# Kernel tuning notes

Hardware: AMD Instinct MI355X
Metric: run time of the kernel (lower is better)

Reference implementation:

```python
import jax, jax.numpy as jnp
import numpy as np

B, S, H = 2, 2048, 2048
NH, NKV, HD = 16, 4, 128
THETA = 10000.0


def _rope_cos_sin(seq_len, head_dim, theta, dtype):
    inv_freq = 1.0 / (theta ** (jnp.arange(0, head_dim, 2, dtype=jnp.float32) / head_dim))
    t = jnp.arange(seq_len, dtype=jnp.float32)
    freqs = t[:, None] * inv_freq[None, :]          # [S, HD/2]
    emb = jnp.concatenate([freqs, freqs], axis=-1)  # [S, HD]
    return jnp.cos(emb).astype(dtype), jnp.sin(emb).astype(dtype)


def _rotate_half(x):
    d = x.shape[-1] // 2
    return jnp.concatenate([-x[..., d:], x[..., :d]], axis=-1)


def setup_inputs() -> dict:
    key = jax.random.key(0)
    ks = jax.random.split(key, 5)
    x = jax.random.normal(ks[0], (B, S, H), dtype=jnp.float32)
    Wq = jax.random.normal(ks[1], (NH * HD, H), dtype=jnp.float32) * 0.02
    Wk = jax.random.normal(ks[2], (NKV * HD, H), dtype=jnp.float32) * 0.02
    Wv = jax.random.normal(ks[3], (NKV * HD, H), dtype=jnp.float32) * 0.02
    Wo = jax.random.normal(ks[4], (H, H), dtype=jnp.float32) * 0.02
    causal = jnp.tril(jnp.ones((S, S), dtype=bool))
    attention_mask = jnp.where(causal, 0.0, -1e9).astype(jnp.float32)[None, None]  # [1,1,S,S]
    return {"x": x, "attention_mask": attention_mask, "Wq": Wq, "Wk": Wk, "Wv": Wv, "Wo": Wo}


def reference(x, attention_mask, Wq, Wk, Wv, Wo):
    b, s, _ = x.shape
    q = (x @ Wq.T).reshape(b, s, NH, HD).transpose(0, 2, 1, 3)    # [b,nh,s,hd]
    k = (x @ Wk.T).reshape(b, s, NKV, HD).transpose(0, 2, 1, 3)   # [b,nkv,s,hd]
    v = (x @ Wv.T).reshape(b, s, NKV, HD).transpose(0, 2, 1, 3)
    cos, sin = _rope_cos_sin(s, HD, THETA, x.dtype)               # [s,hd] each
    cos = cos[None, None]; sin = sin[None, None]
    q = q * cos + _rotate_half(q) * sin
    k = k * cos + _rotate_half(k) * sin
    rep = NH // NKV
    k = jnp.repeat(k, rep, axis=1)                                 # [b,nh,s,hd]
    v = jnp.repeat(v, rep, axis=1)
    scores = jnp.einsum('bhqd,bhkd->bhqk', q, k) / jnp.sqrt(jnp.asarray(HD, x.dtype))
    scores = scores + attention_mask
    attn = jax.nn.softmax(scores, axis=-1)
    out = jnp.einsum('bhqk,bhkd->bhqd', attn, v)                   # [b,nh,s,hd]
    out = out.transpose(0, 2, 1, 3).reshape(b, s, NH * HD)
    return out @ Wo.T
```

## Files before the change

### kernel.cpp

```cpp
#include <hip/hip_runtime.h>

typedef unsigned short u16;
typedef __bf16 bf16x8 __attribute__((ext_vector_type(8)));
typedef float f32x4 __attribute__((ext_vector_type(4)));

#define S_LEN  2048
#define NHEADS 16
#define NKVH   4
#define HDIM   128
#define BB     2
#define MROWS  4096
#define QKV_N  3072
#define HID    2048

__device__ __forceinline__ u16 f2b(float f) {
  union { float f; unsigned u; } x; x.f = f;
  unsigned r = x.u + 0x7fffu + ((x.u >> 16) & 1u);
  return (u16)(r >> 16);
}
__device__ __forceinline__ u16 f2b_fast(float f) {
  union { float f; unsigned u; } x; x.f = f;
  return (u16)((x.u + 0x8000u) >> 16);
}
__device__ __forceinline__ float b2f(u16 v) {
  union { unsigned u; float f; } x; x.u = ((unsigned)v) << 16;
  return x.f;
}
__device__ __forceinline__ void gload_lds16(const u16* g, u16* l) {
  __builtin_amdgcn_global_load_lds((__attribute__((address_space(1))) void*)g,
                                   (__attribute__((address_space(3))) void*)l,
                                   16, 0, 0);
}

#define PB_X   8192
#define PB_WQ  (PB_X + 4096)
#define PB_WK  (PB_WQ + 1024)
#define PB_WV  (PB_WK + 1024)
#define PB_WO  (PB_WV + 4096)
#define PB_CS  (PB_WO + 512)
__global__ void k_prep(const float* __restrict__ x,
                       const float* __restrict__ Wq, const float* __restrict__ Wk,
                       const float* __restrict__ Wv, const float* __restrict__ Wo,
                       u16* __restrict__ xb, u16* __restrict__ Wqkvb,
                       u16* __restrict__ Wob, float* __restrict__ cs)
{
  const int bid = blockIdx.x, tid = threadIdx.x;
  const float* src; u16* dst; int i;
  if (bid < PB_X)       { i = bid * 256 + tid;            src = x;  dst = xb; }
  else if (bid < PB_WQ) { i = (bid - PB_X) * 256 + tid;   src = Wq; dst = Wqkvb; }
  else if (bid < PB_WK) { i = (bid - PB_WQ) * 256 + tid;  src = Wk; dst = Wqkvb + (size_t)2048 * HID; }
  else if (bid < PB_WV) { i = (bid - PB_WK) * 256 + tid;  src = Wv; dst = Wqkvb + (size_t)2560 * HID; }
  else if (bid < PB_WO) { i = (bid - PB_WV) * 256 + tid;  src = Wo; dst = Wob; }
  else {
    const int p = (bid - PB_WO) * 256 + tid;
    const int s = p >> 6, j = p & 63;
    float inv = expf(-(float)j * 0.14391156831212787f);
    float ang = (float)s * inv;
    float c, sn; sincosf(ang, &sn, &c);
    cs[p * 2 + 0] = c; cs[p * 2 + 1] = sn;
    return;
  }
  float4 v = ((const float4*)src)[i];
  ushort4 o;
  o.x = f2b(v.x); o.y = f2b(v.y); o.z = f2b(v.z); o.w = f2b(v.w);
  ((ushort4*)dst)[i] = o;
}

template <int OUT_BF16>
__global__ __launch_bounds__(256) void k_gemm_bt(
    const u16* __restrict__ A, const u16* __restrict__ Bm, void* __restrict__ Cv,
    int M, int N, int K)
{
  __shared__ u16 Al[128 * 32];
  __shared__ u16 Bl[128 * 32];
  const int tid = threadIdx.x;
  const int wave = tid >> 6, lane = tid & 63;
  const int l15 = lane & 15, l4 = lane >> 4;
  const int wr = wave >> 1, wc = wave & 1;
  const int row0 = blockIdx.y * 128, col0 = blockIdx.x * 128;

  f32x4 zero = {0.f, 0.f, 0.f, 0.f};
  f32x4 acc[4][4];
#pragma unroll
  for (int m = 0; m < 4; ++m)
#pragma unroll
    for (int n = 0; n < 4; ++n) acc[m][n] = zero;

  const int e0 = lane * 8;
  for (int kb = 0; kb < K; kb += 32) {
#pragma unroll
    for (int it = 0; it < 2; ++it) {
      const int chunk = it * 4 + wave;
      const int e = chunk * 512 + e0;
      const int r = e >> 5, c = e & 31;
      gload_lds16(A + (size_t)(row0 + r) * K + kb + c, Al + chunk * 512);
      gload_lds16(Bm + (size_t)(col0 + r) * K + kb + c, Bl + chunk * 512);
    }
    __syncthreads();
    bf16x8 af[4], bfv[4];
#pragma unroll
    for (int m = 0; m < 4; ++m)
      af[m] = *(const bf16x8*)(Al + (wr * 64 + m * 16 + l15) * 32 + l4 * 8);
#pragma unroll
    for (int n = 0; n < 4; ++n)
      bfv[n] = *(const bf16x8*)(Bl + (wc * 64 + n * 16 + l15) * 32 + l4 * 8);
#pragma unroll
    for (int m = 0; m < 4; ++m)
#pragma unroll
      for (int n = 0; n < 4; ++n)
        acc[m][n] = __builtin_amdgcn_mfma_f32_16x16x32_bf16(af[m], bfv[n], acc[m][n], 0, 0, 0);
    __syncthreads();
  }
#pragma unroll
  for (int m = 0; m < 4; ++m) {
    const int r = row0 + wr * 64 + m * 16 + l4 * 4;
#pragma unroll
    for (int n = 0; n < 4; ++n) {
      const int c = col0 + wc * 64 + n * 16 + l15;
#pragma unroll
      for (int j = 0; j < 4; ++j) {
        const float v = acc[m][n][j];
        if (OUT_BF16) ((u16*)Cv)[(size_t)(r + j) * N + c] = f2b(v);
        else          ((float*)Cv)[(size_t)(r + j) * N + c] = v;
      }
    }
  }
}

__global__ __launch_bounds__(256) void k_ropev(
    const u16* __restrict__ qkv, const float* __restrict__ cs,
    u16* __restrict__ Qr, u16* __restrict__ Kr, u16* __restrict__ Vt)
{
  const int blk = blockIdx.x;
  const int b = blk >> 8, s0 = (blk & 255) << 3;
  const int tid = threadIdx.x;
  const float S2 = 0.08838834764831845f * 1.4426950408889634f;
#pragma unroll
  for (int p = tid; p < 8192; p += 256) {
    const int s = p >> 10, rem = p & 1023, h = rem >> 6, j = rem & 63;
    const int sg = s0 + s;
    const float c = cs[(sg * 64 + j) * 2], sn = cs[(sg * 64 + j) * 2 + 1];
    const u16* src = qkv + (size_t)(b * S_LEN + sg) * QKV_N + h * 128;
    const float x0 = b2f(src[j]), x1 = b2f(src[64 + j]);
    const size_t base = ((size_t)(b * NHEADS + h) * S_LEN + sg) * HDIM;
    Qr[base + j]      = f2b((x0 * c - x1 * sn) * S2);
    Qr[base + 64 + j] = f2b((x1 * c + x0 * sn) * S2);
  }
#pragma unroll
  for (int p = tid; p < 2048; p += 256) {
    const int s = p >> 8, rem = p & 255, h = rem >> 6, j = rem & 63;
    const int sg = s0 + s;
    const float c = cs[(sg * 64 + j) * 2], sn = cs[(sg * 64 + j) * 2 + 1];
    const u16* src = qkv + (size_t)(b * S_LEN + sg) * QKV_N + 2048 + h * 128;
    const float x0 = b2f(src[j]), x1 = b2f(src[64 + j]);
    const size_t base = ((size_t)(b * NKVH + h) * S_LEN + sg) * HDIM;
    Kr[base + j]      = f2b(x0 * c - x1 * sn);
    Kr[base + 64 + j] = f2b(x1 * c + x0 * sn);
  }
#pragma unroll
  for (int vi = 0; vi < 2; ++vi) {
    const int idx = vi * 256 + tid, h = idx >> 7, d = idx & 127;
    union { u16 u[8]; uint4 v; } bb;
#pragma unroll
    for (int s = 0; s < 8; ++s)
      bb.u[s] = qkv[(size_t)(b * S_LEN + s0 + s) * QKV_N + 2560 + idx];
    *(uint4*)(Vt + ((size_t)(b * NKVH + h) * HDIM + d) * S_LEN + s0) = bb.v;
  }
}

__device__ __forceinline__ void attn_qtile(
    int qt, int lastPhase,
    const u16* __restrict__ Q, const u16* __restrict__ Kg, const u16* __restrict__ Vg,
    u16* __restrict__ Out, int bh,
    u16* Kl0, u16* Kl1, u16* Vl0, u16* Vl1, char* Pb,
    const int (&ko)[4], const int (&vo)[4],
    int wave, int lane, int& cur)
{
  const int l15 = lane & 15, l4 = lane >> 4;
  const int b = bh >> 4, h = bh & 15;
  const int qw0 = qt * 64 + wave * 16;
  const u16* Qg = Q + ((size_t)bh * S_LEN + qw0) * HDIM;

  bf16x8 qf[4];
#pragma unroll
  for (int kc = 0; kc < 4; ++kc)
    qf[kc] = *(const bf16x8*)(Qg + l15 * HDIM + kc * 32 + l4 * 8);

  f32x4 zero = {0.f, 0.f, 0.f, 0.f};
  f32x4 oacc[8];
#pragma unroll
  for (int i = 0; i < 8; ++i) oacc[i] = zero;
  float m_r[4], l_p[4];
#pragma unroll
  for (int j = 0; j < 4; ++j) { m_r[j] = -1e30f; l_p[j] = 0.f; }

  const int nt = qt + 1;

  for (int t = 0; t < nt; ++t) {
    const int kt = t * 64;
    u16* Vb = cur ? Vl1 : Vl0;
#pragma unroll
    for (int it = 0; it < 4; ++it)
      gload_lds16(Vg + (size_t)vo[it] + kt, Vb + (it * 4 + wave) * 512);
    const int hasNext = (t + 1 < nt) || (!lastPhase);
    const int ktn = (t + 1 < nt) ? kt + 64 : 0;
    u16* Kn = cur ? Kl0 : Kl1;
    if (hasNext) {
#pragma unroll
      for (int it = 0; it < 4; ++it)
        gload_lds16(Kg + (size_t)ktn * HDIM + ko[it], Kn + (it * 4 + wave) * 512);
      asm volatile("s_waitcnt vmcnt(8)" ::: "memory");
    } else {
      asm volatile("s_waitcnt vmcnt(4)" ::: "memory");
    }
    __builtin_amdgcn_sched_barrier(0);
    __builtin_amdgcn_s_barrier();
    __builtin_amdgcn_sched_barrier(0);

    const char* Kb = (const char*)(cur ? Kl1 : Kl0);
    {
      f32x4 s[4];
#pragma unroll
      for (int n = 0; n < 4; ++n) s[n] = zero;
      __builtin_amdgcn_s_setprio(1);
#pragma unroll
      for (int n = 0; n < 4; ++n) {
        const int row = n * 16 + l15;
#pragma unroll
        for (int kc = 0; kc < 4; ++kc) {
          const int ab = (row * 256 + kc * 64 + l4 * 16) ^ ((row & 7) << 4);
          bf16x8 kf = *(const bf16x8*)(Kb + ab);
          s[n] = __builtin_amdgcn_mfma_f32_16x16x32_bf16(qf[kc], kf, s[n], 0, 0, 0);
        }
      }
      __builtin_amdgcn_s_setprio(0);
      float sv[4][4], pm[4];
      if (kt + 63 > qw0) {
#pragma unroll
        for (int j = 0; j < 4; ++j) {
          const int qg = qw0 + l4 * 4 + j;
#pragma unroll
          for (int n = 0; n < 4; ++n) {
            float x = s[n][j];
            if (kt + n * 16 + l15 > qg) x = -1e30f;
            sv[n][j] = x;
          }
        }
      } else {
#pragma unroll
        for (int j = 0; j < 4; ++j)
#pragma unroll
          for (int n = 0; n < 4; ++n) sv[n][j] = s[n][j];
      }
#pragma unroll
      for (int j = 0; j < 4; ++j)
        pm[j] = fmaxf(fmaxf(sv[0][j], sv[1][j]), fmaxf(sv[2][j], sv[3][j]));
      bool ok = true;
#pragma unroll
      for (int j = 0; j < 4; ++j) ok = ok && (pm[j] <= m_r[j] + 11.5416f);
      if (!__all(ok)) {
#pragma unroll
        for (int off = 1; off < 16; off <<= 1)
#pragma unroll
          for (int j = 0; j < 4; ++j)
            pm[j] = fmaxf(pm[j], __shfl_xor(pm[j], off, 64));
        float sc[4];
#pragma unroll
        for (int j = 0; j < 4; ++j) {
          const float mn = fmaxf(m_r[j], pm[j]);
          sc[j] = exp2f(m_r[j] - mn);
          m_r[j] = mn;
          l_p[j] *= sc[j];
        }
#pragma unroll
        for (int nd = 0; nd < 8; ++nd)
#pragma unroll
          for (int j = 0; j < 4; ++j) oacc[nd][j] *= sc[j];
      }
#pragma unroll
      for (int n = 0; n < 4; ++n)
#pragma unroll
        for (int j = 0; j < 4; ++j) {
          const float p = exp2f(sv[n][j] - m_r[j]);
          l_p[j] += p;
          const int prow = l4 * 4 + j;
          const int pb = (prow * 128 + (n * 16 + l15) * 2) ^ ((prow & 7) << 4);
          *(u16*)(Pb + pb) = f2b_fast(p);
        }
    }
    if (hasNext) asm volatile("s_waitcnt vmcnt(4)" ::: "memory");
    else         asm volatile("s_waitcnt vmcnt(0)" ::: "memory");
    __builtin_amdgcn_sched_barrier(0);
    __builtin_amdgcn_s_barrier();
    __builtin_amdgcn_sched_barrier(0);
    {
      __builtin_amdgcn_s_setprio(1);
#pragma unroll
      for (int kc2 = 0; kc2 < 2; ++kc2) {
        const int prow = l15;
        const int pbo = (prow * 128 + kc2 * 64 + l4 * 16) ^ ((prow & 7) << 4);
        bf16x8 pf = *(const bf16x8*)(Pb + pbo);
#pragma unroll
        for (int nd = 0; nd < 8; ++nd) {
          const int d = nd * 16 + l15;
          const int ab = (d * 128 + kc2 * 64 + l4 * 16) ^ ((d & 7) << 4);
          bf16x8 vf = *(const bf16x8*)((const char*)Vb + ab);
          oacc[nd] = __builtin_amdgcn_mfma_f32_16x16x32_bf16(pf, vf, oacc[nd], 0, 0, 0);
        }
      }
      __builtin_amdgcn_s_setprio(0);
    }
    cur ^= 1;
  }

#pragma unroll
  for (int off = 1; off < 16; off <<= 1)
#pragma unroll
    for (int j = 0; j < 4; ++j)
      l_p[j] += __shfl_xor(l_p[j], off, 64);
  float il[4];
#pragma unroll
  for (int j = 0; j < 4; ++j) il[j] = 1.f / l_p[j];
  const size_t obase = ((size_t)b * S_LEN + qw0 + l4 * 4) * HID + h * HDIM;
#pragma unroll
  for (int nd = 0; nd < 8; ++nd)
#pragma unroll
    for (int j = 0; j < 4; ++j)
      Out[obase + (size_t)j * HID + nd * 16 + l15] = f2b(oacc[nd][j] * il[j]);
}

__global__ __launch_bounds__(256) void k_attn(
    const u16* __restrict__ Q, const u16* __restrict__ Kr,
    const u16* __restrict__ Vt, u16* __restrict__ Out)
{
  __shared__ u16 Kl[2][64 * 128];
  __shared__ u16 Vl[2][128 * 64];
  __shared__ u16 Pl[4][16 * 64];
  const int tid = threadIdx.x;
  const int wave = tid >> 6, lane = tid & 63;
  const int bh = blockIdx.x;
  const int pairi = blockIdx.y;
  const int b = bh >> 4, h = bh & 15;
  const int kvh = h >> 2;

  const u16* Kg = Kr + (size_t)(b * NKVH + kvh) * S_LEN * HDIM;
  const u16* Vg = Vt + (size_t)(b * NKVH + kvh) * HDIM * S_LEN;

  int ko[4], vo[4];
#pragma unroll
  for (int it = 0; it < 4; ++it) {
    const int c = it * 4 + wave;
    const int L = c * 1024 + lane * 16;
    const int r = L >> 8;  const int w2 = (L & 255) ^ ((r & 7) << 4);
    ko[it] = r * HDIM + (w2 >> 1);
    const int d = L >> 7;  const int wv = (L & 127) ^ ((d & 7) << 4);
    vo[it] = d * S_LEN + (wv >> 1);
  }
#pragma unroll
  for (int it = 0; it < 4; ++it)
    gload_lds16(Kg + ko[it], &Kl[0][(it * 4 + wave) * 512]);

  char* Pb = (char*)&Pl[wave][0];
  int cur = 0;
  attn_qtile(31 - pairi, 0, Q, Kg, Vg, Out, bh, &Kl[0][0], &Kl[1][0],
             &Vl[0][0], &Vl[1][0], Pb, ko, vo, wave, lane, cur);
  attn_qtile(pairi,      1, Q, Kg, Vg, Out, bh, &Kl[0][0], &Kl[1][0],
             &Vl[0][0], &Vl[1][0], Pb, ko, vo, wave, lane, cur);
}

extern "C" void kernel_launch(void* const* d_in, const int* in_sizes, int n_in,
                              void* d_out, int out_size, void* d_ws, size_t ws_size,
                              hipStream_t stream)
{
  const float* x  = (const float*)d_in[0];
  const float* Wq = (const float*)d_in[2];
  const float* Wk = (const float*)d_in[3];
  const float* Wv = (const float*)d_in[4];
  const float* Wo = (const float*)d_in[5];
  float* out = (float*)d_out;

  u16* xb    = (u16*)d_ws;
  u16* Wqkvb = xb    + (size_t)MROWS * HID;
  u16* Wob   = Wqkvb + (size_t)QKV_N * HID;
  u16* qkv   = Wob   + (size_t)HID * HID;
  u16* Qr    = qkv   + (size_t)MROWS * QKV_N;
  u16* Kr    = Qr    + (size_t)BB * NHEADS * S_LEN * HDIM;
  u16* Vt    = Kr    + (size_t)BB * NKVH * S_LEN * HDIM;
  u16* attn  = Vt    + (size_t)BB * NKVH * S_LEN * HDIM;
  float* cs  = (float*)(attn + (size_t)MROWS * HID);

  k_prep<<<dim3(PB_CS), 256, 0, stream>>>(x, Wq, Wk, Wv, Wo, xb, Wqkvb, Wob, cs);
  k_gemm_bt<1><<<dim3(QKV_N / 128, MROWS / 128), 256, 0, stream>>>(xb, Wqkvb, qkv, MROWS, QKV_N, HID);
  k_ropev<<<dim3(BB * 256), 256, 0, stream>>>(qkv, cs, Qr, Kr, Vt);
  k_attn<<<dim3(BB * NHEADS, 16), 256, 0, stream>>>(Qr, Kr, Vt, attn);
  k_gemm_bt<0><<<dim3(HID / 128, MROWS / 128), 256, 0, stream>>>(attn, Wob, out, MROWS, HID, HID);
}
```

Measured before the change: 235.4 us.

## Keep attention probabilities in registers by computing transposed QK^T scores

Swaps the MFMA operands so that S^T is computed, putting each lane on a single query row. The softmax P values can then be packed directly into registers as the A operand of 16x16x16 bf16 MFMAs for PV, instead of going through a per-wave LDS buffer. The row max and sum reductions shrink to two cross-lane shuffles, and packed bf16 conversion uses v_cvt_pk_bf16_f32. The trade-off is twice as many, smaller MFMAs for PV, narrower 8-byte V reads, and extra shuffles to broadcast the rescale factors.

```diff
diff --git a/kernel.cpp b/kernel.cpp
--- a/kernel.cpp
+++ b/kernel.cpp
@@ -3,6 +3,7 @@
 typedef unsigned short u16;
 typedef __bf16 bf16x8 __attribute__((ext_vector_type(8)));
 typedef float f32x4 __attribute__((ext_vector_type(4)));
+typedef short s16x4 __attribute__((ext_vector_type(4)));
 
 #define S_LEN  2048
 #define NHEADS 16
@@ -18,10 +19,6 @@
   unsigned r = x.u + 0x7fffu + ((x.u >> 16) & 1u);
   return (u16)(r >> 16);
 }
-__device__ __forceinline__ u16 f2b_fast(float f) {
-  union { float f; unsigned u; } x; x.f = f;
-  return (u16)((x.u + 0x8000u) >> 16);
-}
 __device__ __forceinline__ float b2f(u16 v) {
   union { unsigned u; float f; } x; x.u = ((unsigned)v) << 16;
   return x.f;
@@ -31,6 +28,23 @@
                                    (__attribute__((address_space(3))) void*)l,
                                    16, 0, 0);
 }
+__device__ __forceinline__ unsigned cvtpk(float lo, float hi) {
+  unsigned r;
+  asm("v_cvt_pk_bf16_f32 %0, %1, %2" : "=v"(r) : "v"(lo), "v"(hi));
+  return r;
+}
+#if __has_builtin(__builtin_amdgcn_mfma_f32_16x16x16bf16_1k)
+__device__ __forceinline__ f32x4 mfma16(s16x4 a, s16x4 b, f32x4 c) {
+  return __builtin_amdgcn_mfma_f32_16x16x16bf16_1k(a, b, c, 0, 0, 0);
+}
+#else
+__device__ __forceinline__ f32x4 mfma16(s16x4 a, s16x4 b, f32x4 c) {
+  f32x4 d;
+  asm volatile("v_mfma_f32_16x16x16_bf16 %0, %1, %2, %3"
+               : "=v"(d) : "v"(a), "v"(b), "v"(c));
+  return d;
+}
+#endif
 
 #define PB_X   8192
 #define PB_WQ  (PB_X + 4096)
@@ -172,7 +186,7 @@
     int qt, int lastPhase,
     const u16* __restrict__ Q, const u16* __restrict__ Kg, const u16* __restrict__ Vg,
     u16* __restrict__ Out, int bh,
-    u16* Kl0, u16* Kl1, u16* Vl0, u16* Vl1, char* Pb,
+    u16* Kl0, u16* Kl1, u16* Vl0, u16* Vl1,
     const int (&ko)[4], const int (&vo)[4],
     int wave, int lane, int& cur)
 {
@@ -190,11 +204,10 @@
   f32x4 oacc[8];
 #pragma unroll
   for (int i = 0; i < 8; ++i) oacc[i] = zero;
-  float m_r[4], l_p[4];
-#pragma unroll
-  for (int j = 0; j < 4; ++j) { m_r[j] = -1e30f; l_p[j] = 0.f; }
+  float m_r = -1e30f, l_p = 0.f;
 
   const int nt = qt + 1;
+  const int qg = qw0 + l15;
 
   for (int t = 0; t < nt; ++t) {
     const int kt = t * 64;
@@ -218,109 +231,94 @@
     __builtin_amdgcn_sched_barrier(0);
 
     const char* Kb = (const char*)(cur ? Kl1 : Kl0);
-    {
-      f32x4 s[4];
-#pragma unroll
-      for (int n = 0; n < 4; ++n) s[n] = zero;
-      __builtin_amdgcn_s_setprio(1);
-#pragma unroll
-      for (int n = 0; n < 4; ++n) {
-        const int row = n * 16 + l15;
-#pragma unroll
-        for (int kc = 0; kc < 4; ++kc) {
-          const int ab = (row * 256 + kc * 64 + l4 * 16) ^ ((row & 7) << 4);
-          bf16x8 kf = *(const bf16x8*)(Kb + ab);
-          s[n] = __builtin_amdgcn_mfma_f32_16x16x32_bf16(qf[kc], kf, s[n], 0, 0, 0);
+    f32x4 s[4];
+#pragma unroll
+    for (int n = 0; n < 4; ++n) s[n] = zero;
+    __builtin_amdgcn_s_setprio(1);
+#pragma unroll
+    for (int n = 0; n < 4; ++n) {
+      const int row = n * 16 + l15;
+#pragma unroll
+      for (int kc = 0; kc < 4; ++kc) {
+        const int ab = (row * 256 + kc * 64 + l4 * 16) ^ ((row & 7) << 4);
+        bf16x8 kf = *(const bf16x8*)(Kb + ab);
+        s[n] = __builtin_amdgcn_mfma_f32_16x16x32_bf16(kf, qf[kc], s[n], 0, 0, 0);
+      }
+    }
+    __builtin_amdgcn_s_setprio(0);
+    float sv[4][4];
+    if (kt + 63 > qw0) {
+#pragma unroll
+      for (int n = 0; n < 4; ++n)
+#pragma unroll
+        for (int j = 0; j < 4; ++j) {
+          float x = s[n][j];
+          if (kt + n * 16 + l4 * 4 + j > qg) x = -1e30f;
+          sv[n][j] = x;
         }
-      }
-      __builtin_amdgcn_s_setprio(0);
-      float sv[4][4], pm[4];
-      if (kt + 63 > qw0) {
-#pragma unroll
-        for (int j = 0; j < 4; ++j) {
-          const int qg = qw0 + l4 * 4 + j;
-#pragma unroll
-          for (int n = 0; n < 4; ++n) {
-            float x = s[n][j];
-            if (kt + n * 16 + l15 > qg) x = -1e30f;
-            sv[n][j] = x;
-          }
-        }
-      } else {
-#pragma unroll
-        for (int j = 0; j < 4; ++j)
-#pragma unroll
-          for (int n = 0; n < 4; ++n) sv[n][j] = s[n][j];
-      }
-#pragma unroll
-      for (int j = 0; j < 4; ++j)
-        pm[j] = fmaxf(fmaxf(sv[0][j], sv[1][j]), fmaxf(sv[2][j], sv[3][j]));
-      bool ok = true;
-#pragma unroll
-      for (int j = 0; j < 4; ++j) ok = ok && (pm[j] <= m_r[j] + 11.5416f);
-      if (!__all(ok)) {
-#pragma unroll
-        for (int off = 1; off < 16; off <<= 1)
-#pragma unroll
-          for (int j = 0; j < 4; ++j)
-            pm[j] = fmaxf(pm[j], __shfl_xor(pm[j], off, 64));
-        float sc[4];
-#pragma unroll
-        for (int j = 0; j < 4; ++j) {
-          const float mn = fmaxf(m_r[j], pm[j]);
-          sc[j] = exp2f(m_r[j] - mn);
-          m_r[j] = mn;
-          l_p[j] *= sc[j];
-        }
-#pragma unroll
-        for (int nd = 0; nd < 8; ++nd)
-#pragma unroll
-          for (int j = 0; j < 4; ++j) oacc[nd][j] *= sc[j];
-      }
+    } else {
 #pragma unroll
       for (int n = 0; n < 4; ++n)
 #pragma unroll
-        for (int j = 0; j < 4; ++j) {
-          const float p = exp2f(sv[n][j] - m_r[j]);
-          l_p[j] += p;
-          const int prow = l4 * 4 + j;
-          const int pb = (prow * 128 + (n * 16 + l15) * 2) ^ ((prow & 7) << 4);
-          *(u16*)(Pb + pb) = f2b_fast(p);
-        }
+        for (int j = 0; j < 4; ++j) sv[n][j] = s[n][j];
+    }
+    float pm = sv[0][0];
+#pragma unroll
+    for (int n = 0; n < 4; ++n)
+#pragma unroll
+      for (int j = 0; j < 4; ++j) pm = fmaxf(pm, sv[n][j]);
+    if (!__all(pm <= m_r + 11.5416f)) {
+      float pf = fmaxf(pm, __shfl_xor(pm, 16, 64));
+      pf = fmaxf(pf, __shfl_xor(pf, 32, 64));
+      const float mn = fmaxf(m_r, pf);
+      const float sc = exp2f(m_r - mn);
+      m_r = mn;
+      l_p *= sc;
+      float scq[4];
+#pragma unroll
+      for (int j = 0; j < 4; ++j) scq[j] = __shfl(sc, l4 * 4 + j, 64);
+#pragma unroll
+      for (int nd = 0; nd < 8; ++nd)
+#pragma unroll
+        for (int j = 0; j < 4; ++j) oacc[nd][j] *= scq[j];
+    }
+    union { unsigned u[2]; s16x4 v; } a[4];
+#pragma unroll
+    for (int n = 0; n < 4; ++n) {
+      const float p0 = exp2f(sv[n][0] - m_r);
+      const float p1 = exp2f(sv[n][1] - m_r);
+      const float p2 = exp2f(sv[n][2] - m_r);
+      const float p3 = exp2f(sv[n][3] - m_r);
+      l_p += (p0 + p1) + (p2 + p3);
+      a[n].u[0] = cvtpk(p0, p1);
+      a[n].u[1] = cvtpk(p2, p3);
     }
     if (hasNext) asm volatile("s_waitcnt vmcnt(4)" ::: "memory");
     else         asm volatile("s_waitcnt vmcnt(0)" ::: "memory");
     __builtin_amdgcn_sched_barrier(0);
     __builtin_amdgcn_s_barrier();
     __builtin_amdgcn_sched_barrier(0);
-    {
-      __builtin_amdgcn_s_setprio(1);
-#pragma unroll
-      for (int kc2 = 0; kc2 < 2; ++kc2) {
-        const int prow = l15;
-        const int pbo = (prow * 128 + kc2 * 64 + l4 * 16) ^ ((prow & 7) << 4);
-        bf16x8 pf = *(const bf16x8*)(Pb + pbo);
-#pragma unroll
-        for (int nd = 0; nd < 8; ++nd) {
-          const int d = nd * 16 + l15;
-          const int ab = (d * 128 + kc2 * 64 + l4 * 16) ^ ((d & 7) << 4);
-          bf16x8 vf = *(const bf16x8*)((const char*)Vb + ab);
-          oacc[nd] = __builtin_amdgcn_mfma_f32_16x16x32_bf16(pf, vf, oacc[nd], 0, 0, 0);
-        }
+    __builtin_amdgcn_s_setprio(1);
+#pragma unroll
+    for (int nd = 0; nd < 8; ++nd) {
+      const int d = nd * 16 + l15;
+      const int rowb = d * 128, swz = (d & 7) << 4;
+#pragma unroll
+      for (int n = 0; n < 4; ++n) {
+        const int ab = (rowb + n * 32 + l4 * 8) ^ swz;
+        s16x4 vf = *(const s16x4*)((const char*)Vb + ab);
+        oacc[nd] = mfma16(a[n].v, vf, oacc[nd]);
       }
-      __builtin_amdgcn_s_setprio(0);
-    }
+    }
+    __builtin_amdgcn_s_setprio(0);
     cur ^= 1;
   }
 
-#pragma unroll
-  for (int off = 1; off < 16; off <<= 1)
-#pragma unroll
-    for (int j = 0; j < 4; ++j)
-      l_p[j] += __shfl_xor(l_p[j], off, 64);
+  l_p += __shfl_xor(l_p, 16, 64);
+  l_p += __shfl_xor(l_p, 32, 64);
   float il[4];
 #pragma unroll
-  for (int j = 0; j < 4; ++j) il[j] = 1.f / l_p[j];
+  for (int j = 0; j < 4; ++j) il[j] = 1.f / __shfl(l_p, l4 * 4 + j, 64);
   const size_t obase = ((size_t)b * S_LEN + qw0 + l4 * 4) * HID + h * HDIM;
 #pragma unroll
   for (int nd = 0; nd < 8; ++nd)
@@ -335,7 +333,6 @@
 {
   __shared__ u16 Kl[2][64 * 128];
   __shared__ u16 Vl[2][128 * 64];
-  __shared__ u16 Pl[4][16 * 64];
   const int tid = threadIdx.x;
   const int wave = tid >> 6, lane = tid & 63;
   const int bh = blockIdx.x;
@@ -360,12 +357,11 @@
   for (int it = 0; it < 4; ++it)
     gload_lds16(Kg + ko[it], &Kl[0][(it * 4 + wave) * 512]);
 
-  char* Pb = (char*)&Pl[wave][0];
   int cur = 0;
   attn_qtile(31 - pairi, 0, Q, Kg, Vg, Out, bh, &Kl[0][0], &Kl[1][0],
-             &Vl[0][0], &Vl[1][0], Pb, ko, vo, wave, lane, cur);
+             &Vl[0][0], &Vl[1][0], ko, vo, wave, lane, cur);
   attn_qtile(pairi,      1, Q, Kg, Vg, Out, bh, &Kl[0][0], &Kl[1][0],
-             &Vl[0][0], &Vl[1][0], Pb, ko, vo, wave, lane, cur);
+             &Vl[0][0], &Vl[1][0], ko, vo, wave, lane, cur);
 }
 
 extern "C" void kernel_launch(void* const* d_in, const int* in_sizes, int n_in,
```

Measured after the change: 231.5 us. No clear change (-1.6%).
